# Kernel tuning notes

Measured on AMD Instinct MI355X. Metric: run time of the kernel, lower is better.

## Reference

```python
import jax, jax.numpy as jnp
import numpy as np

NEG = -9e15
ALPHA = 0.2  # leaky relu slope

def setup_inputs() -> dict:
    key = jax.random.key(0)
    k1, k2, k3, k4 = jax.random.split(key, 4)
    N, Fin, Fout = 8192, 512, 256
    h = jax.random.normal(k1, (N, Fin), dtype=jnp.float32)
    adj = jax.random.randint(k2, (N, N), 0, 2, dtype=jnp.int32)
    # xavier_uniform with gain=1.414
    gain = 1.414
    limW = gain * np.sqrt(6.0 / (Fin + Fout))
    W = jax.random.uniform(k3, (Fin, Fout), dtype=jnp.float32, minval=-limW, maxval=limW)
    lima = gain * np.sqrt(6.0 / (2 * Fout + 1))
    a = jax.random.uniform(k4, (2 * Fout, 1), dtype=jnp.float32, minval=-lima, maxval=lima)
    return {"h": h, "adj": adj, "W": W, "a": a}

def reference(h, adj, W, a):
    Fout = W.shape[1]
    Wh = h @ W                                   # [N, Fout]
    # decompose a = [a1; a2]: e_ij = leaky(a1.Wh_i + a2.Wh_j)
    f1 = Wh @ a[:Fout]                           # [N, 1]
    f2 = Wh @ a[Fout:]                           # [N, 1]
    e = jax.nn.leaky_relu(f1 + f2.T, negative_slope=ALPHA)  # [N, N]
    e = jnp.where(adj > 0, e, jnp.float32(NEG))
    attention = jax.nn.softmax(e, axis=1)
    # dropout is identity at inference (training=False)
    h_prime = attention @ Wh                     # [N, Fout]
    return jax.nn.elu(h_prime)
```

## Files before the change

### kernel.cpp

```cpp
#include <hip/hip_runtime.h>
#include <cstdint>
#include <cstddef>

#define ALPHA 0.2f

typedef __attribute__((ext_vector_type(8)))  short short8;
typedef __attribute__((ext_vector_type(16))) float f32x16;

static __device__ __forceinline__ unsigned short f2bf(float x) {
  union { float f; unsigned u; } c; c.f = x;
  unsigned u = c.u;
  unsigned r = (u + 0x7FFFu + ((u >> 16) & 1u)) >> 16;
  return (unsigned short)r;
}

__global__ __launch_bounds__(512) void gemm1(const float* __restrict__ h,
                                             const float* __restrict__ W,
                                             float* __restrict__ Wh) {
  __shared__ float As[32][132];
  __shared__ float Bs[32][64];
  const int t = threadIdx.x;
  const int bid = blockIdx.x;
  const int nb = bid & 3, mb = bid >> 2;
  const int m0 = mb * 128, n0 = nb * 64;
  const int ty = t >> 4, tx = t & 15;
  float acc[4][4];
#pragma unroll
  for (int i = 0; i < 4; i++)
#pragma unroll
    for (int j = 0; j < 4; j++) acc[i][j] = 0.f;

  for (int k0 = 0; k0 < 512; k0 += 32) {
#pragma unroll
    for (int c = 0; c < 2; c++) {
      int m = c * 64 + (t >> 3);
      int kq = (t & 7) * 4;
      float4 v = *(const float4*)&h[(size_t)(m0 + m) * 512 + k0 + kq];
      As[kq + 0][m] = v.x; As[kq + 1][m] = v.y;
      As[kq + 2][m] = v.z; As[kq + 3][m] = v.w;
    }
    {
      int k = t >> 4;
      int n = (t & 15) * 4;
      *(float4*)&Bs[k][n] = *(const float4*)&W[(size_t)(k0 + k) * 256 + n0 + n];
    }
    __syncthreads();
#pragma unroll
    for (int k = 0; k < 32; k++) {
      float4 a = *(float4*)&As[k][ty * 4];
      float4 b = *(float4*)&Bs[k][tx * 4];
      float av[4] = {a.x, a.y, a.z, a.w};
      float bv[4] = {b.x, b.y, b.z, b.w};
#pragma unroll
      for (int i = 0; i < 4; i++)
#pragma unroll
        for (int j = 0; j < 4; j++) acc[i][j] = fmaf(av[i], bv[j], acc[i][j]);
    }
    __syncthreads();
  }
#pragma unroll
  for (int i = 0; i < 4; i++) {
    float4 v = {acc[i][0], acc[i][1], acc[i][2], acc[i][3]};
    *(float4*)&Wh[(size_t)(m0 + ty * 4 + i) * 256 + n0 + tx * 4] = v;
  }
}

__global__ __launch_bounds__(256) void rowstats(const float* __restrict__ Wh,
                                                const float* __restrict__ a,
                                                float* __restrict__ f1,
                                                float* __restrict__ f2,
                                                unsigned* __restrict__ uvpack) {
  const int t = threadIdx.x;
  const int w = t >> 6, lane = t & 63;
  const int i = blockIdx.x * 4 + w;
  float4 wv = *(const float4*)&Wh[(size_t)i * 256 + lane * 4];
  float4 a1 = *(const float4*)&a[lane * 4];
  float4 a2 = *(const float4*)&a[256 + lane * 4];
  float s1 = wv.x * a1.x + wv.y * a1.y + wv.z * a1.z + wv.w * a1.w;
  float s2 = wv.x * a2.x + wv.y * a2.y + wv.z * a2.z + wv.w * a2.w;
#pragma unroll
  for (int off = 32; off; off >>= 1) { s1 += __shfl_xor(s1, off); s2 += __shfl_xor(s2, off); }
  if (lane == 0) {
    f1[i] = s1; f2[i] = s2;
    float u = __expf(s2), v = __expf(ALPHA * s2);
    uvpack[i] = (unsigned)f2bf(u) | ((unsigned)f2bf(v) << 16);
  }
}

__global__ __launch_bounds__(256) void wtrans(const float* __restrict__ Wh,
                                              unsigned short* __restrict__ WhT) {
  __shared__ unsigned short T[64][80];
  const int t = threadIdx.x;
  const int bi = blockIdx.x & 127;
  const int bc = blockIdx.x >> 7;
  const int i0 = bi * 64, c0 = bc * 64;
  {
    const int il = t >> 2, cq = (t & 3) * 16;
#pragma unroll
    for (int k = 0; k < 4; ++k) {
      float4 v = *(const float4*)&Wh[(size_t)(i0 + il) * 256 + c0 + cq + k * 4];
      T[cq + k * 4 + 0][il] = f2bf(v.x);
      T[cq + k * 4 + 1][il] = f2bf(v.y);
      T[cq + k * 4 + 2][il] = f2bf(v.z);
      T[cq + k * 4 + 3][il] = f2bf(v.w);
    }
  }
  __syncthreads();
  {
    const int cl = t >> 2, iq = (t & 3) * 16;
    *(uint4*)&WhT[(size_t)(c0 + cl) * 8192 + i0 + iq]     = *(const uint4*)&T[cl][iq];
    *(uint4*)&WhT[(size_t)(c0 + cl) * 8192 + i0 + iq + 8] = *(const uint4*)&T[cl][iq + 8];
  }
}

__global__ __launch_bounds__(256) void f2max_k(const float* __restrict__ f2,
                                               float* __restrict__ f2maxp) {
  __shared__ float red[256];
  const int t = threadIdx.x;
  float m = -1e30f;
  for (int c = 0; c < 32; c++) m = fmaxf(m, f2[c * 256 + t]);
  red[t] = m;
  __syncthreads();
  for (int s = 128; s; s >>= 1) {
    if (t < s) red[t] = fmaxf(red[t], red[t + s]);
    __syncthreads();
  }
  if (t == 0) f2maxp[0] = red[0];
}

__global__ __launch_bounds__(256) void maskpack(const int* __restrict__ adj,
                                                unsigned long long* __restrict__ mask) {
  __shared__ unsigned long long mbuf[4][128];
  const int t = threadIdx.x, wave = t >> 6, lane = t & 63;
  const int row = blockIdx.x * 4 + wave;
  const int* ap = adj + (size_t)row * 8192 + lane;
#pragma unroll 1
  for (int it0 = 0; it0 < 128; it0 += 4) {
    int a0 = ap[(it0 + 0) * 64];
    int a1 = ap[(it0 + 1) * 64];
    int a2 = ap[(it0 + 2) * 64];
    int a3 = ap[(it0 + 3) * 64];
    unsigned long long b0 = __ballot(a0 > 0);
    unsigned long long b1 = __ballot(a1 > 0);
    unsigned long long b2 = __ballot(a2 > 0);
    unsigned long long b3 = __ballot(a3 > 0);
    if (lane == 0) {
      mbuf[wave][it0 + 0] = b0; mbuf[wave][it0 + 1] = b1;
      mbuf[wave][it0 + 2] = b2; mbuf[wave][it0 + 3] = b3;
    }
  }
  __syncthreads();
  uint4* dst = (uint4*)(mask + (size_t)blockIdx.x * 4 * 128);
  dst[t] = ((const uint4*)mbuf)[t];
}

#define ATTN_SUB(KSUB, MWORD, UCA, UCB, BFC, BFN, SCUR)                          \
  {                                                                              \
    const unsigned mbyte_ = ((MWORD) >> (((KSUB) & 1) * 16 + aselsh)) & 0xFFu;   \
    const unsigned uu_[8] = {UCA.x, UCA.y, UCA.z, UCA.w, UCB.x, UCB.y, UCB.z, UCB.w}; \
    float w_[8];                                                                 \
    _Pragma("unroll")                                                            \
    for (int jj = 0; jj < 8; jj++) {                                             \
      union { unsigned u; float f; } cu_, cv_;                                   \
      cu_.u = uu_[jj] << 16;                                                     \
      cv_.u = uu_[jj] & 0xFFFF0000u;                                             \
      float wv_ = (cu_.f > Ui) ? Ai * cu_.f : Bi * cv_.f;                        \
      int ext_ = ((int)(mbyte_ << (31 - jj))) >> 31;    \
      union { float f; int i; } wu_; wu_.f = wv_; wu_.i &= ext_;                 \
      w_[jj] = wu_.f;                                                            \
    }                                                                            \
    lpriv += ((w_[0] + w_[1]) + (w_[2] + w_[3])) + ((w_[4] + w_[5]) + (w_[6] + w_[7])); \
    union { uint4 q; short8 s; } af_;                                            \
    asm("v_cvt_pk_bf16_f32 %0, %1, %2" : "=v"(af_.q.x) : "v"(w_[0]), "v"(w_[1]));\
    asm("v_cvt_pk_bf16_f32 %0, %1, %2" : "=v"(af_.q.y) : "v"(w_[2]), "v"(w_[3]));\
    asm("v_cvt_pk_bf16_f32 %0, %1, %2" : "=v"(af_.q.z) : "v"(w_[4]), "v"(w_[5]));\
    asm("v_cvt_pk_bf16_f32 %0, %1, %2" : "=v"(af_.q.w) : "v"(w_[6]), "v"(w_[7]));\
    const int sn_ = (SCUR) + 1 < 128 ? (SCUR) + 1 : 127;                         \
    _Pragma("unroll")                                                            \
    for (int ct = 0; ct < 8; ct++)                                               \
      BFN[ct] = *(const short8*)(wtp + (size_t)ct * (32 * 8192) + (size_t)sn_ * 16); \
    _Pragma("unroll")                                                            \
    for (int ct = 0; ct < 8; ct++)                                               \
      acc[ct] = __builtin_amdgcn_mfma_f32_32x32x16_bf16(af_.s, BFC[ct], acc[ct], 0, 0, 0); \
  }

#define ATTN_GROUP(G, UC, UN, MC, MN)                                            \
  {                                                                              \
    const int gn_ = (G) < 31 ? (G) + 1 : 31;                                     \
    MN = mp[gn_];                                                                \
    UN[0] = *(const uint4*)(uvp + gn_ * 64 + 0);                                 \
    UN[1] = *(const uint4*)(uvp + gn_ * 64 + 4);                                 \
    ATTN_SUB(0, MC.x, UC[0], UC[1], bfA, bfB, 4 * (G) + 0);                      \
    UN[2] = *(const uint4*)(uvp + gn_ * 64 + 16);                                \
    UN[3] = *(const uint4*)(uvp + gn_ * 64 + 20);                                \
    ATTN_SUB(1, MC.x, UC[2], UC[3], bfB, bfA, 4 * (G) + 1);                      \
    UN[4] = *(const uint4*)(uvp + gn_ * 64 + 32);                                \
    UN[5] = *(const uint4*)(uvp + gn_ * 64 + 36);                                \
    ATTN_SUB(2, MC.y, UC[4], UC[5], bfA, bfB, 4 * (G) + 2);                      \
    UN[6] = *(const uint4*)(uvp + gn_ * 64 + 48);                                \
    UN[7] = *(const uint4*)(uvp + gn_ * 64 + 52);                                \
    ATTN_SUB(3, MC.y, UC[6], UC[7], bfB, bfA, 4 * (G) + 3);                      \
  }

__global__ __launch_bounds__(256, 1) void attn_main(const unsigned long long* __restrict__ maskw,
                                                    const float* __restrict__ f1,
                                                    const unsigned* __restrict__ uvpack,
                                                    const unsigned short* __restrict__ WhT,
                                                    const float* __restrict__ f2maxp,
                                                    float* __restrict__ out) {
  __shared__ float red[4][32][260];
  __shared__ float lsum[4][32];
  const int t = threadIdx.x;
  const int wave = t >> 6, lane = t & 63;
  const int am = lane & 31, asel = lane >> 5;
  const int aselsh = asel * 8;
  const int r0 = blockIdx.x * 32;
  const int row = r0 + am;
  const int jq = wave * 2048;

  const float F2max = f2maxp[0];
  const float f1v = f1[row];
  const float x = f1v + F2max;
  const float M = x > 0.f ? x : ALPHA * x;
  const float Ai = __expf(f1v - M);
  const float Bi = __expf(ALPHA * f1v - M);
  const float Ui = __expf(-f1v);

  f32x16 acc[8] = {};
  const uint2* mp = (const uint2*)maskw + (size_t)row * 128 + wave * 32;
  const unsigned* uvp = uvpack + jq + aselsh;
  const unsigned short* wtp = WhT + (size_t)am * 8192 + jq + aselsh;

  uint2 mg = mp[0], mgN;
  uint4 ug[8], ugN[8];
#pragma unroll
  for (int k = 0; k < 4; k++) {
    ug[2 * k]     = *(const uint4*)(uvp + k * 16);
    ug[2 * k + 1] = *(const uint4*)(uvp + k * 16 + 4);
  }
  short8 bfA[8], bfB[8];
#pragma unroll
  for (int ct = 0; ct < 8; ct++)
    bfA[ct] = *(const short8*)(wtp + (size_t)ct * (32 * 8192));
  float lpriv = 0.f;

#pragma unroll 1
  for (int gg = 0; gg < 16; ++gg) {
    ATTN_GROUP(2 * gg,     ug,  ugN, mg,  mgN);
    ATTN_GROUP(2 * gg + 1, ugN, ug,  mgN, mg);
  }

#pragma unroll
  for (int ct = 0; ct < 8; ct++) {
#pragma unroll
    for (int reg = 0; reg < 16; reg++) {
      const int rowl = (reg & 3) + 8 * (reg >> 2) + 4 * asel;
      red[wave][rowl][ct * 32 + am] = acc[ct][reg];
    }
  }
  lpriv += __shfl_xor(lpriv, 32);
  if (asel == 0) lsum[wave][am] = lpriv;
  __syncthreads();

  const int rr = t >> 3, cb = (t & 7) * 32;
  const float l = lsum[0][rr] + lsum[1][rr] + lsum[2][rr] + lsum[3][rr];
  const float inv = 1.0f / fmaxf(l, 1e-30f);
#pragma unroll
  for (int cc = 0; cc < 32; cc += 4) {
    float4 v;
    v.x = red[0][rr][cb + cc + 0] + red[1][rr][cb + cc + 0] + red[2][rr][cb + cc + 0] + red[3][rr][cb + cc + 0];
    v.y = red[0][rr][cb + cc + 1] + red[1][rr][cb + cc + 1] + red[2][rr][cb + cc + 1] + red[3][rr][cb + cc + 1];
    v.z = red[0][rr][cb + cc + 2] + red[1][rr][cb + cc + 2] + red[2][rr][cb + cc + 2] + red[3][rr][cb + cc + 2];
    v.w = red[0][rr][cb + cc + 3] + red[1][rr][cb + cc + 3] + red[2][rr][cb + cc + 3] + red[3][rr][cb + cc + 3];
    v.x *= inv; v.y *= inv; v.z *= inv; v.w *= inv;
    float4 o;
    o.x = v.x > 0.f ? v.x : __expf(v.x) - 1.f;
    o.y = v.y > 0.f ? v.y : __expf(v.y) - 1.f;
    o.z = v.z > 0.f ? v.z : __expf(v.z) - 1.f;
    o.w = v.w > 0.f ? v.w : __expf(v.w) - 1.f;
    *(float4*)&out[(size_t)(r0 + rr) * 256 + cb + cc] = o;
  }
}

extern "C" void kernel_launch(void* const* d_in, const int* in_sizes, int n_in,
                              void* d_out, int out_size, void* d_ws, size_t ws_size,
                              hipStream_t stream) {
  const float* h  = (const float*)d_in[0];
  const int* adj  = (const int*)d_in[1];
  const float* W  = (const float*)d_in[2];
  const float* a  = (const float*)d_in[3];
  float* out = (float*)d_out;
  char* ws = (char*)d_ws;

  float* Wh            = (float*)ws;
  unsigned long long* mask = (unsigned long long*)(ws + (size_t)(8u << 20));
  unsigned short* WhT  = (unsigned short*)(ws + (size_t)(16u << 20));
  float* f1            = (float*)(ws + (size_t)(20u << 20));
  float* f2            = (float*)(ws + (size_t)(20u << 20) + (32u << 10));
  unsigned* uvpack     = (unsigned*)(ws + (size_t)(20u << 20) + (64u << 10));
  float* f2maxp        = (float*)(ws + (size_t)(20u << 20) + (96u << 10));

  maskpack<<<2048, 256, 0, stream>>>(adj, mask);
  gemm1<<<256, 512, 0, stream>>>(h, W, Wh);
  rowstats<<<2048, 256, 0, stream>>>(Wh, a, f1, f2, uvpack);
  wtrans<<<512, 256, 0, stream>>>(Wh, WhT);
  f2max_k<<<1, 256, 0, stream>>>(f2, f2maxp);
  attn_main<<<256, 256, 0, stream>>>(mask, f1, uvpack, WhT, f2maxp, out);
}
```

Before: 548.9 us.

## Split attention work across column groups and j-halves; shrink gemm1 tiles

```diff
diff --git a/kernel.cpp b/kernel.cpp
--- a/kernel.cpp
+++ b/kernel.cpp
@@ -14,15 +14,15 @@
   return (unsigned short)r;
 }
 
-__global__ __launch_bounds__(512) void gemm1(const float* __restrict__ h,
-                                             const float* __restrict__ W,
-                                             float* __restrict__ Wh) {
-  __shared__ float As[32][132];
+__global__ __launch_bounds__(256, 2) void gemm1(const float* __restrict__ h,
+                                                const float* __restrict__ W,
+                                                float* __restrict__ Wh) {
+  __shared__ float As[32][68];
   __shared__ float Bs[32][64];
   const int t = threadIdx.x;
   const int bid = blockIdx.x;
   const int nb = bid & 3, mb = bid >> 2;
-  const int m0 = mb * 128, n0 = nb * 64;
+  const int m0 = mb * 64, n0 = nb * 64;
   const int ty = t >> 4, tx = t & 15;
   float acc[4][4];
 #pragma unroll
@@ -33,14 +33,15 @@
   for (int k0 = 0; k0 < 512; k0 += 32) {
 #pragma unroll
     for (int c = 0; c < 2; c++) {
-      int m = c * 64 + (t >> 3);
+      int m = c * 32 + (t >> 3);
       int kq = (t & 7) * 4;
       float4 v = *(const float4*)&h[(size_t)(m0 + m) * 512 + k0 + kq];
       As[kq + 0][m] = v.x; As[kq + 1][m] = v.y;
       As[kq + 2][m] = v.z; As[kq + 3][m] = v.w;
     }
-    {
-      int k = t >> 4;
+#pragma unroll
+    for (int c = 0; c < 2; c++) {
+      int k = c * 16 + (t >> 4);
       int n = (t & 15) * 4;
       *(float4*)&Bs[k][n] = *(const float4*)&W[(size_t)(k0 + k) * 256 + n0 + n];
     }
@@ -175,18 +176,20 @@
     asm("v_cvt_pk_bf16_f32 %0, %1, %2" : "=v"(af_.q.y) : "v"(w_[2]), "v"(w_[3]));\
     asm("v_cvt_pk_bf16_f32 %0, %1, %2" : "=v"(af_.q.z) : "v"(w_[4]), "v"(w_[5]));\
     asm("v_cvt_pk_bf16_f32 %0, %1, %2" : "=v"(af_.q.w) : "v"(w_[6]), "v"(w_[7]));\
-    const int sn_ = (SCUR) + 1 < 128 ? (SCUR) + 1 : 127;                         \
-    _Pragma("unroll")                                                            \
-    for (int ct = 0; ct < 8; ct++)                                               \
-      BFN[ct] = *(const short8*)(wtp + (size_t)ct * (32 * 8192) + (size_t)sn_ * 16); \
-    _Pragma("unroll")                                                            \
-    for (int ct = 0; ct < 8; ct++)                                               \
-      acc[ct] = __builtin_amdgcn_mfma_f32_32x32x16_bf16(af_.s, BFC[ct], acc[ct], 0, 0, 0); \
+    const int sn_ = (SCUR) + 1 < 256 ? (SCUR) + 1 : 255;                         \
+    BFN[0] = *(const short8*)(wtp0 + (size_t)0 * (32 * 8192) + (size_t)sn_ * 16);\
+    BFN[1] = *(const short8*)(wtp0 + (size_t)1 * (32 * 8192) + (size_t)sn_ * 16);\
+    BFN[2] = *(const short8*)(wtp0 + (size_t)2 * (32 * 8192) + (size_t)sn_ * 16);\
+    BFN[3] = *(const short8*)(wtp0 + (size_t)3 * (32 * 8192) + (size_t)sn_ * 16);\
+    acc[0] = __builtin_amdgcn_mfma_f32_32x32x16_bf16(af_.s, BFC[0], acc[0], 0, 0, 0); \
+    acc[1] = __builtin_amdgcn_mfma_f32_32x32x16_bf16(af_.s, BFC[1], acc[1], 0, 0, 0); \
+    acc[2] = __builtin_amdgcn_mfma_f32_32x32x16_bf16(af_.s, BFC[2], acc[2], 0, 0, 0); \
+    acc[3] = __builtin_amdgcn_mfma_f32_32x32x16_bf16(af_.s, BFC[3], acc[3], 0, 0, 0); \
   }
 
 #define ATTN_GROUP(G, UC, UN, MC, MN)                                            \
   {                                                                              \
-    const int gn_ = (G) < 31 ? (G) + 1 : 31;                                     \
+    const int gn_ = (G) < 63 ? (G) + 1 : 63;                                     \
     MN = mp[gn_];                                                                \
     UN[0] = *(const uint4*)(uvp + gn_ * 64 + 0);                                 \
     UN[1] = *(const uint4*)(uvp + gn_ * 64 + 4);                                 \
@@ -208,15 +211,15 @@
                                                     const unsigned short* __restrict__ WhT,
                                                     const float* __restrict__ f2maxp,
                                                     float* __restrict__ out) {
-  __shared__ float red[4][32][260];
-  __shared__ float lsum[4][32];
+  __shared__ float red[2][32][260];
+  __shared__ float lsum[2][32];
   const int t = threadIdx.x;
   const int wave = t >> 6, lane = t & 63;
+  const int cg = wave >> 1, jh = wave & 1;
   const int am = lane & 31, asel = lane >> 5;
   const int aselsh = asel * 8;
   const int r0 = blockIdx.x * 32;
   const int row = r0 + am;
-  const int jq = wave * 2048;
 
   const float F2max = f2maxp[0];
   const float f1v = f1[row];
@@ -226,10 +229,10 @@
   const float Bi = __expf(ALPHA * f1v - M);
   const float Ui = __expf(-f1v);
 
-  f32x16 acc[8] = {};
-  const uint2* mp = (const uint2*)maskw + (size_t)row * 128 + wave * 32;
-  const unsigned* uvp = uvpack + jq + aselsh;
-  const unsigned short* wtp = WhT + (size_t)am * 8192 + jq + aselsh;
+  f32x16 acc[4] = {};
+  const uint2* mp = (const uint2*)maskw + (size_t)row * 128 + jh * 64;
+  const unsigned* uvp = uvpack + jh * 4096 + aselsh;
+  const unsigned short* wtp0 = WhT + (size_t)(cg * 128 + am) * 8192 + jh * 4096 + aselsh;
 
   uint2 mg = mp[0], mgN;
   uint4 ug[8], ugN[8];
@@ -238,40 +241,40 @@
     ug[2 * k]     = *(const uint4*)(uvp + k * 16);
     ug[2 * k + 1] = *(const uint4*)(uvp + k * 16 + 4);
   }
-  short8 bfA[8], bfB[8];
-#pragma unroll
-  for (int ct = 0; ct < 8; ct++)
-    bfA[ct] = *(const short8*)(wtp + (size_t)ct * (32 * 8192));
+  short8 bfA[4], bfB[4];
+#pragma unroll
+  for (int ct = 0; ct < 4; ct++)
+    bfA[ct] = *(const short8*)(wtp0 + (size_t)ct * (32 * 8192));
   float lpriv = 0.f;
 
 #pragma unroll 1
-  for (int gg = 0; gg < 16; ++gg) {
+  for (int gg = 0; gg < 32; ++gg) {
     ATTN_GROUP(2 * gg,     ug,  ugN, mg,  mgN);
     ATTN_GROUP(2 * gg + 1, ugN, ug,  mgN, mg);
   }
 
 #pragma unroll
-  for (int ct = 0; ct < 8; ct++) {
+  for (int ct = 0; ct < 4; ct++) {
 #pragma unroll
     for (int reg = 0; reg < 16; reg++) {
       const int rowl = (reg & 3) + 8 * (reg >> 2) + 4 * asel;
-      red[wave][rowl][ct * 32 + am] = acc[ct][reg];
+      red[jh][rowl][cg * 128 + ct * 32 + am] = acc[ct][reg];
     }
   }
   lpriv += __shfl_xor(lpriv, 32);
-  if (asel == 0) lsum[wave][am] = lpriv;
+  if (cg == 0 && asel == 0) lsum[jh][am] = lpriv;
   __syncthreads();
 
   const int rr = t >> 3, cb = (t & 7) * 32;
-  const float l = lsum[0][rr] + lsum[1][rr] + lsum[2][rr] + lsum[3][rr];
+  const float l = lsum[0][rr] + lsum[1][rr];
   const float inv = 1.0f / fmaxf(l, 1e-30f);
 #pragma unroll
   for (int cc = 0; cc < 32; cc += 4) {
     float4 v;
-    v.x = red[0][rr][cb + cc + 0] + red[1][rr][cb + cc + 0] + red[2][rr][cb + cc + 0] + red[3][rr][cb + cc + 0];
-    v.y = red[0][rr][cb + cc + 1] + red[1][rr][cb + cc + 1] + red[2][rr][cb + cc + 1] + red[3][rr][cb + cc + 1];
-    v.z = red[0][rr][cb + cc + 2] + red[1][rr][cb + cc + 2] + red[2][rr][cb + cc + 2] + red[3][rr][cb + cc + 2];
-    v.w = red[0][rr][cb + cc + 3] + red[1][rr][cb + cc + 3] + red[2][rr][cb + cc + 3] + red[3][rr][cb + cc + 3];
+    v.x = red[0][rr][cb + cc + 0] + red[1][rr][cb + cc + 0];
+    v.y = red[0][rr][cb + cc + 1] + red[1][rr][cb + cc + 1];
+    v.z = red[0][rr][cb + cc + 2] + red[1][rr][cb + cc + 2];
+    v.w = red[0][rr][cb + cc + 3] + red[1][rr][cb + cc + 3];
     v.x *= inv; v.y *= inv; v.z *= inv; v.w *= inv;
     float4 o;
     o.x = v.x > 0.f ? v.x : __expf(v.x) - 1.f;
@@ -301,7 +304,7 @@
   float* f2maxp        = (float*)(ws + (size_t)(20u << 20) + (96u << 10));
 
   maskpack<<<2048, 256, 0, stream>>>(adj, mask);
-  gemm1<<<256, 512, 0, stream>>>(h, W, Wh);
+  gemm1<<<512, 256, 0, stream>>>(h, W, Wh);
   rowstats<<<2048, 256, 0, stream>>>(Wh, a, f1, f2, uvpack);
   wtrans<<<512, 256, 0, stream>>>(Wh, WhT);
   f2max_k<<<1, 256, 0, stream>>>(f2, f2maxp);
```

Result: no change. 554.8 us (+1.1%).
